# Optimization experiments

Measured on AMD Instinct MI355X. Metric: run time of the kernel, lower is better.

The kernel has to match this reference:

```python
import jax, jax.numpy as jnp
import numpy as np

NUM = 8          # nlk*nlk - 1
IDX_REF = 4      # center neighbor index


def _gather2d(img, yi, xi):
    # img: (B,H,W); yi,xi: int32 (B,K,H,W) already clipped in-range
    B, H, W = img.shape
    flat = img.reshape(B, H * W)
    idx = (yi * W + xi).reshape(B, -1)
    return jnp.take_along_axis(flat, idx, axis=1).reshape(yi.shape)


def _bilinear(img, ys, xs):
    # bilinear sample with zero padding outside (deform-conv v2 semantics)
    # img: (B,H,W); ys,xs: float (B,K,H,W)
    B, H, W = img.shape
    y0 = jnp.floor(ys)
    x0 = jnp.floor(xs)
    y0i = y0.astype(jnp.int32)
    x0i = x0.astype(jnp.int32)
    wy1 = ys - y0
    wx1 = xs - x0
    out = jnp.zeros(ys.shape, img.dtype)
    for dy, wy in ((0, 1.0 - wy1), (1, wy1)):
        for dx, wx in ((0, 1.0 - wx1), (1, wx1)):
            yy = y0i + dy
            xx = x0i + dx
            valid = ((yy >= 0) & (yy < H) & (xx >= 0) & (xx < W)).astype(img.dtype)
            v = _gather2d(img, jnp.clip(yy, 0, H - 1), jnp.clip(xx, 0, W - 1))
            out = out + wy * wx * valid * v
    return out


def _conv3(x, w):
    return jax.lax.conv_general_dilated(x, w, (1, 1), ((1, 1), (1, 1)),
                                        dimension_numbers=('NCHW', 'OIHW', 'NCHW'))


def _bn_relu(x, g, b, m, v):
    s = g / jnp.sqrt(v + 1e-5)
    return jax.nn.relu(x * s[None, :, None, None] + (b - m * s)[None, :, None, None])


def _disp_warp(right, disp):
    # sample right image at x' = x - disparity, bilinear along width, zeros outside
    B, C, H, W = right.shape
    xs = jnp.arange(W, dtype=right.dtype)[None, None, :] - disp[:, 0]  # (B,H,W)
    x0 = jnp.floor(xs)
    x0i = x0.astype(jnp.int32)
    w1 = xs - x0
    out = jnp.zeros_like(right)
    for d, w in ((0, 1.0 - w1), (1, w1)):
        xi = x0i + d
        valid = ((xi >= 0) & (xi < W)).astype(right.dtype)
        v = jnp.take_along_axis(right, jnp.clip(xi, 0, W - 1)[:, None], axis=3)
        out = out + (w * valid)[:, None] * v
    return out


def _forward(coarse_disparity, normal_estimation, left_image, right_image, confidence,
             conv1_w, bn1_g, bn1_b, bn1_m, bn1_v,
             conv2_w, bn2_g, bn2_b, bn2_m, bn2_v,
             conv3_w, aff_scale_const):
    B, _, H, W = coarse_disparity.shape
    # current_scale == 1 => interpolate is identity, disp_ == coarse_disparity
    warped_error = _disp_warp(right_image, coarse_disparity) - left_image
    guidance = jnp.concatenate([normal_estimation, left_image, right_image, warped_error], axis=1)

    x = _bn_relu(_conv3(guidance, conv1_w), bn1_g, bn1_b, bn1_m, bn1_v)
    x = _bn_relu(_conv3(x, conv2_w), bn2_g, bn2_b, bn2_m, bn2_v)
    oa = _conv3(x, conv3_w)                                   # (B, 3*NUM, H, W)

    o1, o2, aff = oa[:, :NUM], oa[:, NUM:2 * NUM], oa[:, 2 * NUM:]
    # torch: cat((o1,o2),1).view(B,NUM,2,H,W) -> faithful pairing of channels
    off = jnp.concatenate([o1, o2], axis=1).reshape(B, NUM, 2, H, W)
    zero_c = jnp.zeros((B, 1, 2, H, W), off.dtype)
    off9 = jnp.concatenate([off[:, :IDX_REF], zero_c, off[:, IDX_REF:]], axis=1)  # (B,9,2,H,W)

    aff = jnp.tanh(aff) / (aff_scale_const + 1e-8)            # TGASS

    # confidence gather at p + offset_k (1x1 deform conv, w_conf=1), offsets detached
    ii = jnp.arange(H, dtype=off.dtype)[None, None, :, None]
    jj = jnp.arange(W, dtype=off.dtype)[None, None, None, :]
    off_nc = jax.lax.stop_gradient(
        jnp.concatenate([off9[:, :IDX_REF], off9[:, IDX_REF + 1:]], axis=1))  # (B,8,2,H,W)
    conf_aff = _bilinear(confidence[:, 0], ii + off_nc[:, :, 0], jj + off_nc[:, :, 1])
    aff = aff * conf_aff

    s = jnp.sum(jnp.abs(aff), axis=1, keepdims=True) + 1e-4
    s = jnp.maximum(s, 1.0)                                   # TGASS clamp
    aff = aff / s
    aff_ref = 1.0 - jnp.sum(aff, axis=1, keepdims=True)
    aff9 = jnp.concatenate([aff[:, :IDX_REF], aff_ref, aff[:, IDX_REF:]], axis=1)  # (B,9,H,W)

    # one propagation: modulated deformable 3x3 conv, all-ones weight, zero bias
    ky = (jnp.arange(9, dtype=off.dtype) // 3 - 1.0)[None, :, None, None]
    kx = (jnp.arange(9, dtype=off.dtype) % 3 - 1.0)[None, :, None, None]
    sampled = _bilinear(coarse_disparity[:, 0], ii + ky + off9[:, :, 0], jj + kx + off9[:, :, 1])
    inter = jnp.sum(aff9 * sampled, axis=1, keepdims=True)    # (B,1,H,W)
    inter = inter * (inter >= 0).astype(inter.dtype)
    inter = jnp.maximum(inter, 0.0)
    final = jnp.maximum(0.7 * coarse_disparity + 0.3 * inter, 0.0)
    return final


def setup_inputs() -> dict:
    key = jax.random.key(0)
    ks = jax.random.split(key, 20)
    B, H, W = 4, 384, 1280
    inp = {}
    inp['coarse_disparity'] = jax.random.uniform(ks[0], (B, 1, H, W), jnp.float32) * 40.0
    inp['normal_estimation'] = jax.random.normal(ks[1], (B, 3, H, W), jnp.float32)
    inp['left_image'] = jax.random.uniform(ks[2], (B, 3, H, W), jnp.float32)
    inp['right_image'] = jax.random.uniform(ks[3], (B, 3, H, W), jnp.float32)
    inp['confidence'] = jax.random.uniform(ks[4], (B, 1, H, W), jnp.float32)
    inp['conv1_w'] = jax.random.normal(ks[5], (32, 12, 3, 3), jnp.float32) * 0.05
    inp['bn1_g'] = jax.random.uniform(ks[6], (32,), jnp.float32) + 0.5
    inp['bn1_b'] = jax.random.normal(ks[7], (32,), jnp.float32) * 0.1
    inp['bn1_m'] = jax.random.normal(ks[8], (32,), jnp.float32) * 0.1
    inp['bn1_v'] = jax.random.uniform(ks[9], (32,), jnp.float32) + 0.5
    inp['conv2_w'] = jax.random.normal(ks[10], (64, 32, 3, 3), jnp.float32) * 0.05
    inp['bn2_g'] = jax.random.uniform(ks[11], (64,), jnp.float32) + 0.5
    inp['bn2_b'] = jax.random.normal(ks[12], (64,), jnp.float32) * 0.1
    inp['bn2_m'] = jax.random.normal(ks[13], (64,), jnp.float32) * 0.1
    inp['bn2_v'] = jax.random.uniform(ks[14], (64,), jnp.float32) + 0.5
    inp['conv3_w'] = jax.random.normal(ks[15], (3 * NUM, 64, 3, 3), jnp.float32) * 0.05
    inp['aff_scale_const'] = jnp.array([1.0 * NUM], jnp.float32)  # affinity_gamma * num
    return inp


def reference(coarse_disparity, normal_estimation, left_image, right_image, confidence,
              conv1_w, bn1_g, bn1_b, bn1_m, bn1_v,
              conv2_w, bn2_g, bn2_b, bn2_m, bn2_v,
              conv3_w, aff_scale_const):
    return _forward(coarse_disparity, normal_estimation, left_image, right_image, confidence,
                    conv1_w, bn1_g, bn1_b, bn1_m, bn1_v,
                    conv2_w, bn2_g, bn2_b, bn2_m, bn2_v,
                    conv3_w, aff_scale_const)
```

## Files before the change

### kernel.cpp

```cpp
#include <hip/hip_runtime.h>
#include <math.h>

static constexpr int B_ = 4;
static constexpr int H_ = 384;
static constexpr int W_ = 1280;
static constexpr int HW_ = H_ * W_;

typedef _Float16 f16x8 __attribute__((ext_vector_type(8)));
typedef float f32x4 __attribute__((ext_vector_type(4)));


template <int C_IN, int C_OUT>
__global__ __launch_bounds__(256) void prep_w(const float* __restrict__ w,
                                              unsigned short* __restrict__ wb)
{
  constexpr int CICH = C_IN / 32;
  constexpr int NCOT = (C_OUT + 15) / 16;
  constexpr int NE = NCOT * CICH * 9 * 512;
  int i = blockIdx.x * 256 + threadIdx.x;
  if (i >= NE) return;
  int k   = i & 31;
  int row = (i >> 5) & 15;
  int ts  = i >> 9;
  int s   = ts % 9;
  int tc  = ts / 9;
  int c   = tc % CICH;
  int t   = tc / CICH;
  int co  = t * 16 + row;
  int ci  = c * 32 + k;
  float v = 0.f;
  if (co < C_OUT) v = w[((size_t)co * C_IN + ci) * 9 + s];
  union { _Float16 f; unsigned short u; } ch;
  ch.f = (_Float16)v;
  wb[i] = ch.u;
}

__global__ __launch_bounds__(256) void prep_w1(const float* __restrict__ w,
                                               unsigned short* __restrict__ wb)
{
  constexpr int NE = 2 * 6 * 512;
  int i = blockIdx.x * 256 + threadIdx.x;
  if (i >= NE) return;
  int k    = i & 31;
  int row  = (i >> 5) & 15;
  int ts   = i >> 9;
  int chunk = ts % 6;
  int tc   = ts / 6;
  int ky   = chunk >> 1;
  int kc   = chunk & 1;
  int kx, ci;
  bool valid;
  if (kc == 0) { kx = k >> 4;  ci = k & 15; valid = (ci < 12); }
  else         { kx = 2;       ci = k & 15; valid = (k < 16) && (ci < 12); }
  int co = tc * 16 + row;
  float v = valid ? w[((size_t)co * 12 + ci) * 9 + ky * 3 + kx] : 0.f;
  union { _Float16 f; unsigned short u; } ch;
  ch.f = (_Float16)v;
  wb[i] = ch.u;
}

__global__ __launch_bounds__(256, 4) void conv1_mfma(
    const float* __restrict__ disp, const float* __restrict__ normal,
    const float* __restrict__ left, const float* __restrict__ right,
    const unsigned short* __restrict__ wb,
    const float* __restrict__ bn_g, const float* __restrict__ bn_b,
    const float* __restrict__ bn_m, const float* __restrict__ bn_v,
    unsigned short* __restrict__ out,
    int b0, int out_y0, int out_rows)
{
  constexpr int NCOT = 2;
  constexpr int TY  = 8;
  constexpr int HR  = 10;
  constexpr int TXI = 36;

  __shared__ unsigned short smem[HR * TXI * 16];

  const int tilesX = W_ / 32;
  int bb = blockIdx.x;
  const int txi = bb % tilesX; bb /= tilesX;
  const int tilesY = (out_rows + TY - 1) / TY;
  const int tyi = bb % tilesY;
  const int gi  = bb / tilesY;
  const int b   = b0 + gi;
  const int x0  = txi * 32;
  const int oy0 = out_y0 + tyi * TY;

  const int tid    = threadIdx.x;
  const int w      = tid >> 6;
  const int lane15 = tid & 15;
  const int kgrp   = (tid >> 4) & 3;
  const int aoff   = lane15 * 32 + kgrp * 8;

  f32x4 acc[NCOT][2][2];
#pragma unroll
  for (int i = 0; i < NCOT; i++)
#pragma unroll
    for (int rr = 0; rr < 2; rr++) {
      acc[i][rr][0] = (f32x4){0.f, 0.f, 0.f, 0.f};
      acc[i][rr][1] = (f32x4){0.f, 0.f, 0.f, 0.f};
    }

  for (int it = tid; it < HR * TXI; it += 256) {
    int row = it / TXI;
    int px  = it - row * TXI;
    int gy  = oy0 - 1 + row;
    int gx  = x0 - 2 + px;
    union { _Float16 f[16]; uint4 u[2]; } R;
    R.u[0] = (uint4){0, 0, 0, 0};
    R.u[1] = (uint4){0, 0, 0, 0};
    if (((unsigned)gy < (unsigned)H_) & ((unsigned)gx < (unsigned)W_)) {
      size_t p = (size_t)gy * W_ + gx;
      float d = disp[(size_t)b * HW_ + p];
      float xs = (float)gx - d;
      float x0f = floorf(xs);
      int xi0 = (int)x0f;
      float w1 = xs - x0f;
      int xi1 = xi0 + 1;
      float v0 = (xi0 >= 0 && xi0 < W_) ? 1.f : 0.f;
      float v1 = (xi1 >= 0 && xi1 < W_) ? 1.f : 0.f;
      int xc0 = min(max(xi0, 0), W_ - 1);
      int xc1 = min(max(xi1, 0), W_ - 1);
      float w0f = (1.f - w1) * v0;
      float w1f = w1 * v1;
#pragma unroll
      for (int c = 0; c < 3; c++) {
        const float* rrow = right + (size_t)(b * 3 + c) * HW_ + (size_t)gy * W_;
        float l = left[(size_t)(b * 3 + c) * HW_ + p];
        float n = normal[(size_t)(b * 3 + c) * HW_ + p];
        float r = rrow[gx];
        float warped = w0f * rrow[xc0] + w1f * rrow[xc1];
        R.f[c]     = (_Float16)n;
        R.f[3 + c] = (_Float16)l;
        R.f[6 + c] = (_Float16)r;
        R.f[9 + c] = (_Float16)(warped - l);
      }
    }
    unsigned short* dst = &smem[it * 16];
    *(uint4*)(dst)     = R.u[0];
    *(uint4*)(dst + 8) = R.u[1];
  }
  __syncthreads();

  f16x8 ah[NCOT];
#pragma unroll
  for (int tc = 0; tc < NCOT; tc++)
    ah[tc] = *(const f16x8*)(wb + ((size_t)(tc * 6 + 0) * 512 + aoff));
#pragma unroll
  for (int c = 0; c < 6; c++) {
    const int ky = c >> 1, kc = c & 1;
    f16x8 ahn[NCOT];
    if (c < 5) {
#pragma unroll
      for (int tc = 0; tc < NCOT; tc++)
        ahn[tc] = *(const f16x8*)(wb + ((size_t)(tc * 6 + c + 1) * 512 + aoff));
    }
#pragma unroll
    for (int rr = 0; rr < 2; rr++) {
      const int col = (kc ? 3 : 1) + lane15;
      const int e0 = ((2 * w + rr + ky) * TXI + col) * 16 + kgrp * 8;
      f16x8 b0 = *(const f16x8*)&smem[e0];
      f16x8 b1 = *(const f16x8*)&smem[e0 + 256];
#pragma unroll
      for (int tc = 0; tc < NCOT; tc++) {
        acc[tc][rr][0] = __builtin_amdgcn_mfma_f32_16x16x32_f16(
            ah[tc], b0, acc[tc][rr][0], 0, 0, 0);
        acc[tc][rr][1] = __builtin_amdgcn_mfma_f32_16x16x32_f16(
            ah[tc], b1, acc[tc][rr][1], 0, 0, 0);
      }
    }
    if (c < 5) {
#pragma unroll
      for (int tc = 0; tc < NCOT; tc++) ah[tc] = ahn[tc];
    }
  }

#pragma unroll
  for (int rr = 0; rr < 2; rr++) {
    const int orow = oy0 + 2 * w + rr;
    if (orow < out_y0 + out_rows) {
      const int ox = x0 + lane15;
#pragma unroll
      for (int tc = 0; tc < NCOT; tc++) {
        const int o = tc * 2 + (kgrp >> 1);
        const size_t recbase =
            (((size_t)(gi * 4 + o) * out_rows + (orow - out_y0)) * W_ + ox) * 8
            + (kgrp & 1) * 4;
#pragma unroll
        for (int nt = 0; nt < 2; nt++) {
          union { _Float16 f[4]; uint2 u; } Hh;
#pragma unroll
          for (int j = 0; j < 4; j++) {
            const int co = tc * 16 + kgrp * 4 + j;
            float s = bn_g[co] * rsqrtf(bn_v[co] + 1e-5f);
            float v = fmaxf(acc[tc][rr][nt][j] * s + (bn_b[co] - bn_m[co] * s), 0.f);
            Hh.f[j] = (_Float16)v;
          }
          *(uint2*)&out[recbase + (size_t)nt * 128] = Hh.u;
        }
      }
    }
  }
}

__global__ __launch_bounds__(256, 4) void conv2_mfma(
    const unsigned short* __restrict__ in, const unsigned short* __restrict__ wb,
    const float* __restrict__ bn_g, const float* __restrict__ bn_b,
    const float* __restrict__ bn_m, const float* __restrict__ bn_v,
    unsigned short* __restrict__ out,
    int in_y0, int in_rows, int out_y0, int out_rows)
{
  constexpr int C_IN = 32, C_OUT = 64;
  constexpr int CICH = 1;
  constexpr int NCIO = 4;
  constexpr int NCOT = 4;
  constexpr int TY  = 8;
  constexpr int HR  = 10;
  constexpr int TXI = 36;
  constexpr int PX2 = 18;
  constexpr int PXW = 36;

  __shared__ unsigned short smem[HR * TXI * PXW];

  const int tilesX = W_ / 32;
  int bb = blockIdx.x;
  const int txi = bb % tilesX; bb /= tilesX;
  const int tilesY = (out_rows + TY - 1) / TY;
  const int tyi = bb % tilesY;
  const int gi  = bb / tilesY;
  const int x0  = txi * 32;
  const int oy0 = out_y0 + tyi * TY;

  const int tid    = threadIdx.x;
  const int w      = tid >> 6;
  const int lane15 = tid & 15;
  const int kgrp   = (tid >> 4) & 3;
  const int aoff   = lane15 * 32 + kgrp * 8;

  f32x4 acc[NCOT][2][2];
#pragma unroll
  for (int i = 0; i < NCOT; i++)
#pragma unroll
    for (int rr = 0; rr < 2; rr++) {
      acc[i][rr][0] = (f32x4){0.f, 0.f, 0.f, 0.f};
      acc[i][rr][1] = (f32x4){0.f, 0.f, 0.f, 0.f};
    }

  for (int it = tid; it < 4 * HR * PX2; it += 256) {
    int cib = it / (HR * PX2);
    int pos = it - cib * (HR * PX2);
    int row = pos / PX2;
    int p2  = pos - row * PX2;
    int gy  = oy0 - 1 + row;
    int by  = gy - in_y0;
    int gx  = x0 - 2 + 2 * p2;
    const bool rok = (unsigned)by < (unsigned)in_rows;
    uint4 h0 = {0,0,0,0}, h1 = {0,0,0,0};
    const unsigned short* src =
        in + (((size_t)(gi * NCIO + cib) * in_rows + by) * W_ + gx) * 8;
    if (rok & ((unsigned)gx < (unsigned)W_))       h0 = *(const uint4*)(src);
    if (rok & ((unsigned)(gx + 1) < (unsigned)W_)) h1 = *(const uint4*)(src + 8);
    int base = (row * TXI + 2 * p2) * PXW + cib * 8;
    *(uint4*)&smem[base]       = h0;
    *(uint4*)&smem[base + PXW] = h1;
  }
  __syncthreads();

  f16x8 ah[NCOT];
#pragma unroll
  for (int tc = 0; tc < NCOT; tc++)
    ah[tc] = *(const f16x8*)(wb + ((size_t)(tc * 9) * 512 + aoff));
#pragma unroll
  for (int s = 0; s < 9; s++) {
    const int ky = s / 3, kx = s - 3 * ky;
    f16x8 ahn[NCOT];
    if (s < 8) {
#pragma unroll
      for (int tc = 0; tc < NCOT; tc++)
        ahn[tc] = *(const f16x8*)(wb + ((size_t)(tc * 9 + s + 1) * 512 + aoff));
    }
#pragma unroll
    for (int rr = 0; rr < 2; rr++) {
      const int e0 = ((2 * w + rr + ky) * TXI + 1 + lane15 + kx) * PXW + kgrp * 8;
      f16x8 b0 = *(const f16x8*)&smem[e0];
      f16x8 b1 = *(const f16x8*)&smem[e0 + 16 * PXW];
#pragma unroll
      for (int tc = 0; tc < NCOT; tc++) {
        acc[tc][rr][0] = __builtin_amdgcn_mfma_f32_16x16x32_f16(
            ah[tc], b0, acc[tc][rr][0], 0, 0, 0);
        acc[tc][rr][1] = __builtin_amdgcn_mfma_f32_16x16x32_f16(
            ah[tc], b1, acc[tc][rr][1], 0, 0, 0);
      }
    }
    if (s < 8) {
#pragma unroll
      for (int tc = 0; tc < NCOT; tc++) ah[tc] = ahn[tc];
    }
  }

#pragma unroll
  for (int rr = 0; rr < 2; rr++) {
    const int orow = oy0 + 2 * w + rr;
    if (orow < out_y0 + out_rows) {
      const int ox = x0 + lane15;
#pragma unroll
      for (int tc = 0; tc < NCOT; tc++) {
        const int o = tc * 2 + (kgrp >> 1);
        const size_t recbase =
            (((size_t)(gi * 8 + o) * out_rows + (orow - out_y0)) * W_ + ox) * 8
            + (kgrp & 1) * 4;
#pragma unroll
        for (int nt = 0; nt < 2; nt++) {
          union { _Float16 f[4]; uint2 u; } Hh;
#pragma unroll
          for (int j = 0; j < 4; j++) {
            const int co = tc * 16 + kgrp * 4 + j;
            float s = bn_g[co] * rsqrtf(bn_v[co] + 1e-5f);
            float v = fmaxf(acc[tc][rr][nt][j] * s + (bn_b[co] - bn_m[co] * s), 0.f);
            Hh.f[j] = (_Float16)v;
          }
          *(uint2*)&out[recbase + (size_t)nt * 128] = Hh.u;
        }
      }
    }
  }
}

__device__ __forceinline__ float bilin1(const float* __restrict__ img,
                                        float ys, float xs)
{
  float y0f = floorf(ys), x0f = floorf(xs);
  int y0 = (int)y0f, x0 = (int)x0f;
  float wy1 = ys - y0f, wx1 = xs - x0f;
  float wy0 = 1.f - wy1, wx0 = 1.f - wx1;
  int y1 = y0 + 1, x1 = x0 + 1;
  float vy0 = (y0 >= 0 && y0 < H_) ? 1.f : 0.f;
  float vy1 = (y1 >= 0 && y1 < H_) ? 1.f : 0.f;
  float vx0 = (x0 >= 0 && x0 < W_) ? 1.f : 0.f;
  float vx1 = (x1 >= 0 && x1 < W_) ? 1.f : 0.f;
  int yc0 = min(max(y0, 0), H_ - 1), yc1 = min(max(y1, 0), H_ - 1);
  int xc0 = min(max(x0, 0), W_ - 1), xc1 = min(max(x1, 0), W_ - 1);
  const float* r0 = img + (size_t)yc0 * W_;
  const float* r1 = img + (size_t)yc1 * W_;
  float v00 = r0[xc0], v01 = r0[xc1], v10 = r1[xc0], v11 = r1[xc1];
  return (wy0 * vy0) * ((wx0 * vx0) * v00 + (wx1 * vx1) * v01) +
         (wy1 * vy1) * ((wx0 * vx0) * v10 + (wx1 * vx1) * v11);
}

__global__ __launch_bounds__(256, 4) void conv3_final(
    const unsigned short* __restrict__ in, const unsigned short* __restrict__ wb,
    const float* __restrict__ conf, const float* __restrict__ disp,
    const float* __restrict__ asc, float* __restrict__ outp,
    int b0, int in_y0, int in_rows, int out_y0, int out_rows)
{
  constexpr int NCIO = 8;
  constexpr int CICH = 2;
  constexpr int NCOT = 2;
  constexpr int TY  = 8;
  constexpr int HR  = 10;
  constexpr int TXI = 36;
  constexpr int PX2 = 18;
  constexpr int PXW = 36;
  constexpr int COS = 260;

  __shared__ unsigned short smem[HR * TXI * PXW];
  float* oal = (float*)smem;

  const int tilesX = W_ / 32;
  int bb = blockIdx.x;
  const int txi = bb % tilesX; bb /= tilesX;
  const int tilesY = (out_rows + TY - 1) / TY;
  const int tyi = bb % tilesY;
  const int gi  = bb / tilesY;
  const int b   = b0 + gi;
  const int x0  = txi * 32;
  const int oy0 = out_y0 + tyi * TY;

  const int tid    = threadIdx.x;
  const int w      = tid >> 6;
  const int lane15 = tid & 15;
  const int kgrp   = (tid >> 4) & 3;
  const int aoff   = lane15 * 32 + kgrp * 8;

  f32x4 acc[NCOT][2][2];
#pragma unroll
  for (int i = 0; i < NCOT; i++)
#pragma unroll
    for (int rr = 0; rr < 2; rr++) {
      acc[i][rr][0] = (f32x4){0.f, 0.f, 0.f, 0.f};
      acc[i][rr][1] = (f32x4){0.f, 0.f, 0.f, 0.f};
    }

  for (int cc = 0; cc < CICH; ++cc) {
    if (cc) __syncthreads();
    for (int it = tid; it < 4 * HR * PX2; it += 256) {
      int cib = it / (HR * PX2);
      int pos = it - cib * (HR * PX2);
      int row = pos / PX2;
      int p2  = pos - row * PX2;
      int gy  = oy0 - 1 + row;
      int by  = gy - in_y0;
      int gx  = x0 - 2 + 2 * p2;
      const bool rok = (unsigned)by < (unsigned)in_rows;
      uint4 h0 = {0,0,0,0}, h1 = {0,0,0,0};
      const unsigned short* src =
          in + (((size_t)(gi * NCIO + cc * 4 + cib) * in_rows + by) * W_ + gx) * 8;
      if (rok & ((unsigned)gx < (unsigned)W_))       h0 = *(const uint4*)(src);
      if (rok & ((unsigned)(gx + 1) < (unsigned)W_)) h1 = *(const uint4*)(src + 8);
      int base = (row * TXI + 2 * p2) * PXW + cib * 8;
      *(uint4*)&smem[base]       = h0;
      *(uint4*)&smem[base + PXW] = h1;
    }
    __syncthreads();

    f16x8 ah[NCOT];
#pragma unroll
    for (int tc = 0; tc < NCOT; tc++)
      ah[tc] = *(const f16x8*)(
          wb + ((size_t)((tc * CICH + cc) * 9) * 512 + aoff));
#pragma unroll
    for (int s = 0; s < 9; s++) {
      const int ky = s / 3, kx = s - 3 * ky;
      f16x8 ahn[NCOT];
      if (s < 8) {
#pragma unroll
        for (int tc = 0; tc < NCOT; tc++)
          ahn[tc] = *(const f16x8*)(
              wb + ((size_t)((tc * CICH + cc) * 9 + s + 1) * 512 + aoff));
      }
#pragma unroll
      for (int rr = 0; rr < 2; rr++) {
        const int e0 = ((2 * w + rr + ky) * TXI + 1 + lane15 + kx) * PXW + kgrp * 8;
        f16x8 b0 = *(const f16x8*)&smem[e0];
        f16x8 b1 = *(const f16x8*)&smem[e0 + 16 * PXW];
#pragma unroll
        for (int tc = 0; tc < NCOT; tc++) {
          acc[tc][rr][0] = __builtin_amdgcn_mfma_f32_16x16x32_f16(
              ah[tc], b0, acc[tc][rr][0], 0, 0, 0);
          acc[tc][rr][1] = __builtin_amdgcn_mfma_f32_16x16x32_f16(
              ah[tc], b1, acc[tc][rr][1], 0, 0, 0);
        }
      }
      if (s < 8) {
#pragma unroll
        for (int tc = 0; tc < NCOT; tc++) ah[tc] = ahn[tc];
      }
    }
  }

  __syncthreads();
#pragma unroll
  for (int tc = 0; tc < NCOT; tc++) {
#pragma unroll
    for (int j = 0; j < 4; j++) {
      const int co = tc * 16 + kgrp * 4 + j;
      if (co < 24) {
#pragma unroll
        for (int rr = 0; rr < 2; rr++) {
          const int row = 2 * w + rr;
#pragma unroll
          for (int nt = 0; nt < 2; nt++)
            oal[co * COS + row * 32 + lane15 + nt * 16] = acc[tc][rr][nt][j];
        }
      }
    }
  }
  __syncthreads();

  const int px = tid & 31;
  const int r  = tid >> 5;
  const int orow = oy0 + r;
  const int gx = x0 + px;
  if (orow < out_y0 + out_rows) {
    const float scale = 1.f / (asc[0] + 1e-8f);
    const float* cimg = conf + (size_t)b * HW_;
    const float* dimg = disp + (size_t)b * HW_;
    const int base = r * 32 + px;

    float offy[8], offx[8], a[8];
#pragma unroll
    for (int k = 0; k < 8; k++) {
      offy[k] = oal[(size_t)k * COS + base];
      offx[k] = oal[(size_t)(8 + k) * COS + base];
      float ar = oal[(size_t)(16 + k) * COS + base];
      float ca = bilin1(cimg, (float)orow + offy[k], (float)gx + offx[k]);
      a[k] = tanhf(ar) * scale * ca;
    }

    float s = 1e-4f;
#pragma unroll
    for (int k = 0; k < 8; k++) s += fabsf(a[k]);
    s = fmaxf(s, 1.f);
    float inv = 1.f / s;
    float suma = 0.f;
#pragma unroll
    for (int k = 0; k < 8; k++) { a[k] *= inv; suma += a[k]; }
    float aref = 1.f - suma;

    float inter = 0.f;
#pragma unroll
    for (int k9 = 0; k9 < 9; k9++) {
      float oy, ox, wk;
      if (k9 < 4)       { oy = offy[k9];     ox = offx[k9];     wk = a[k9]; }
      else if (k9 == 4) { oy = 0.f;          ox = 0.f;          wk = aref;  }
      else              { oy = offy[k9 - 1]; ox = offx[k9 - 1]; wk = a[k9 - 1]; }
      float ky = (float)(k9 / 3) - 1.f;
      float kx = (float)(k9 % 3) - 1.f;
      inter += wk * bilin1(dimg, (float)orow + ky + oy, (float)gx + kx + ox);
    }
    inter = fmaxf(inter, 0.f);
    float cd = dimg[(size_t)orow * W_ + gx];
    outp[(size_t)b * HW_ + (size_t)orow * W_ + gx] =
        fmaxf(0.7f * cd + 0.3f * inter, 0.f);
  }
}

extern "C" void kernel_launch(void* const* d_in, const int* in_sizes, int n_in,
                              void* d_out, int out_size, void* d_ws, size_t ws_size,
                              hipStream_t stream)
{
  const float* disp   = (const float*)d_in[0];
  const float* normal = (const float*)d_in[1];
  const float* left   = (const float*)d_in[2];
  const float* right  = (const float*)d_in[3];
  const float* conf   = (const float*)d_in[4];
  const float* w1     = (const float*)d_in[5];
  const float* g1     = (const float*)d_in[6];
  const float* b1     = (const float*)d_in[7];
  const float* m1     = (const float*)d_in[8];
  const float* v1     = (const float*)d_in[9];
  const float* w2     = (const float*)d_in[10];
  const float* g2     = (const float*)d_in[11];
  const float* b2     = (const float*)d_in[12];
  const float* m2     = (const float*)d_in[13];
  const float* v2     = (const float*)d_in[14];
  const float* w3     = (const float*)d_in[15];
  const float* asc    = (const float*)d_in[16];
  float* out = (float*)d_out;

  constexpr int WB1E = 2 * 6 * 512;
  constexpr int WB2E = 4 * 1 * 9 * 512;
  constexpr int WB3E = 2 * 2 * 9 * 512;
  const size_t wbytes = (size_t)(WB1E + WB2E + WB3E) * sizeof(unsigned short);

  struct Cfg { int g, bh; };
  const Cfg cfgs[] = {{4, 384}, {2, 384}, {1, 384}, {4, 96}, {2, 96},
                      {1, 96}, {1, 48}, {1, 24}, {1, 12}, {1, 8}, {1, 4}};
  int G = 1, BH = 4;
  for (const Cfg& c : cfgs) {
    size_t bytes = (size_t)c.g * W_ *
                   (64u * (c.bh + 4) + 128u * (c.bh + 2));
    if (bytes + wbytes <= ws_size) { G = c.g; BH = c.bh; break; }
  }

  unsigned short* x1s = (unsigned short*)d_ws;
  unsigned short* x2s = x1s + (size_t)G * 32 * (BH + 4) * W_;
  unsigned short* wb1 = x2s + (size_t)G * 64 * (BH + 2) * W_;
  unsigned short* wb2 = wb1 + WB1E;
  unsigned short* wb3 = wb2 + WB2E;

  prep_w1<<<(WB1E + 255) / 256, 256, 0, stream>>>(w1, wb1);
  prep_w<32, 64><<<(WB2E + 255) / 256, 256, 0, stream>>>(w2, wb2);
  prep_w<64, 24><<<(WB3E + 255) / 256, 256, 0, stream>>>(w3, wb3);

  const int tilesX = W_ / 32;

  for (int b0 = 0; b0 < B_; b0 += G) {
    for (int y0 = 0; y0 < H_; y0 += BH) {
      const int rows_out = min(BH, H_ - y0);
      const int y_x2_0 = max(y0 - 1, 0);
      const int y_x2_1 = min(y0 + rows_out + 1, H_);
      const int rows_x2 = y_x2_1 - y_x2_0;
      const int y_x1_0 = max(y0 - 2, 0);
      const int y_x1_1 = min(y0 + rows_out + 2, H_);
      const int rows_x1 = y_x1_1 - y_x1_0;

      {
        int grid = tilesX * ((rows_x1 + 7) / 8) * G;
        conv1_mfma<<<grid, 256, 0, stream>>>(
            disp, normal, left, right, wb1, g1, b1, m1, v1, x1s,
            b0, y_x1_0, rows_x1);
      }
      {
        int grid = tilesX * ((rows_x2 + 7) / 8) * G;
        conv2_mfma<<<grid, 256, 0, stream>>>(
            x1s, wb2, g2, b2, m2, v2, x2s,
            y_x1_0, rows_x1, y_x2_0, rows_x2);
      }
      {
        int grid = tilesX * ((rows_out + 7) / 8) * G;
        conv3_final<<<grid, 256, 0, stream>>>(
            x2s, wb3, conf, disp, asc, out,
            b0, y_x2_0, rows_x2, y0, rows_out);
      }
    }
  }
}
```

Before: 560.7 us.

## Fuse conv1 and conv2 into one kernel, keeping conv1 activations in LDS

Merges the conv1 and conv2 kernels so each block computes the conv1 output plus a halo (12x36) into shared memory, then runs conv2 from there. This removes the global write and read of the 32-channel conv1 intermediate and one kernel launch per band. In exchange, the halo rows and columns are recomputed per tile, LDS use rises, and occupancy drops to 3 blocks per CU.

```diff
diff --git a/kernel.cpp b/kernel.cpp
--- a/kernel.cpp
+++ b/kernel.cpp
@@ -59,31 +59,35 @@
   wb[i] = ch.u;
 }
 
-__global__ __launch_bounds__(256, 4) void conv1_mfma(
+__global__ __launch_bounds__(256, 3) void conv12_mfma(
     const float* __restrict__ disp, const float* __restrict__ normal,
     const float* __restrict__ left, const float* __restrict__ right,
-    const unsigned short* __restrict__ wb,
-    const float* __restrict__ bn_g, const float* __restrict__ bn_b,
-    const float* __restrict__ bn_m, const float* __restrict__ bn_v,
+    const unsigned short* __restrict__ wb1, const unsigned short* __restrict__ wb2,
+    const float* __restrict__ g1, const float* __restrict__ b1,
+    const float* __restrict__ m1, const float* __restrict__ v1,
+    const float* __restrict__ g2, const float* __restrict__ b2,
+    const float* __restrict__ m2, const float* __restrict__ v2,
     unsigned short* __restrict__ out,
     int b0, int out_y0, int out_rows)
 {
-  constexpr int NCOT = 2;
-  constexpr int TY  = 8;
-  constexpr int HR  = 10;
-  constexpr int TXI = 36;
-
-  __shared__ unsigned short smem[HR * TXI * 16];
+  constexpr int GW = 52;
+  constexpr int GR = 12;
+  constexpr int XW = 36;
+  constexpr int XR = 12;
+  constexpr int P1 = 2 * 6 * 512;
+
+  __shared__ unsigned short gmem[GR * GW * 16];
+  __shared__ unsigned short xmem[XR * XW * 36];
 
   const int tilesX = W_ / 32;
   int bb = blockIdx.x;
   const int txi = bb % tilesX; bb /= tilesX;
-  const int tilesY = (out_rows + TY - 1) / TY;
+  const int tilesY = (out_rows + 7) / 8;
   const int tyi = bb % tilesY;
   const int gi  = bb / tilesY;
   const int b   = b0 + gi;
   const int x0  = txi * 32;
-  const int oy0 = out_y0 + tyi * TY;
+  const int oy0 = out_y0 + tyi * 8;
 
   const int tid    = threadIdx.x;
   const int w      = tid >> 6;
@@ -91,20 +95,11 @@
   const int kgrp   = (tid >> 4) & 3;
   const int aoff   = lane15 * 32 + kgrp * 8;
 
-  f32x4 acc[NCOT][2][2];
-#pragma unroll
-  for (int i = 0; i < NCOT; i++)
-#pragma unroll
-    for (int rr = 0; rr < 2; rr++) {
-      acc[i][rr][0] = (f32x4){0.f, 0.f, 0.f, 0.f};
-      acc[i][rr][1] = (f32x4){0.f, 0.f, 0.f, 0.f};
-    }
-
-  for (int it = tid; it < HR * TXI; it += 256) {
-    int row = it / TXI;
-    int px  = it - row * TXI;
-    int gy  = oy0 - 1 + row;
-    int gx  = x0 - 2 + px;
+  for (int it = tid; it < GR * GW; it += 256) {
+    int g  = it / GW;
+    int cx = it - g * GW;
+    int gy = oy0 - 2 + g;
+    int gx = x0 - 3 + cx;
     union { _Float16 f[16]; uint4 u[2]; } R;
     R.u[0] = (uint4){0, 0, 0, 0};
     R.u[1] = (uint4){0, 0, 0, 0};
@@ -114,63 +109,146 @@
       float xs = (float)gx - d;
       float x0f = floorf(xs);
       int xi0 = (int)x0f;
-      float w1 = xs - x0f;
+      float w1f_ = xs - x0f;
       int xi1 = xi0 + 1;
-      float v0 = (xi0 >= 0 && xi0 < W_) ? 1.f : 0.f;
-      float v1 = (xi1 >= 0 && xi1 < W_) ? 1.f : 0.f;
+      float vv0 = (xi0 >= 0 && xi0 < W_) ? 1.f : 0.f;
+      float vv1 = (xi1 >= 0 && xi1 < W_) ? 1.f : 0.f;
       int xc0 = min(max(xi0, 0), W_ - 1);
       int xc1 = min(max(xi1, 0), W_ - 1);
-      float w0f = (1.f - w1) * v0;
-      float w1f = w1 * v1;
+      float w0f = (1.f - w1f_) * vv0;
+      float w1f2 = w1f_ * vv1;
 #pragma unroll
       for (int c = 0; c < 3; c++) {
         const float* rrow = right + (size_t)(b * 3 + c) * HW_ + (size_t)gy * W_;
         float l = left[(size_t)(b * 3 + c) * HW_ + p];
         float n = normal[(size_t)(b * 3 + c) * HW_ + p];
         float r = rrow[gx];
-        float warped = w0f * rrow[xc0] + w1f * rrow[xc1];
+        float warped = w0f * rrow[xc0] + w1f2 * rrow[xc1];
         R.f[c]     = (_Float16)n;
         R.f[3 + c] = (_Float16)l;
         R.f[6 + c] = (_Float16)r;
         R.f[9 + c] = (_Float16)(warped - l);
       }
     }
-    unsigned short* dst = &smem[it * 16];
+    unsigned short* dst = &gmem[it * 16];
     *(uint4*)(dst)     = R.u[0];
     *(uint4*)(dst + 8) = R.u[1];
   }
   __syncthreads();
 
-  f16x8 ah[NCOT];
-#pragma unroll
-  for (int tc = 0; tc < NCOT; tc++)
-    ah[tc] = *(const f16x8*)(wb + ((size_t)(tc * 6 + 0) * 512 + aoff));
-#pragma unroll
-  for (int c = 0; c < 6; c++) {
-    const int ky = c >> 1, kc = c & 1;
-    f16x8 ahn[NCOT];
-    if (c < 5) {
-#pragma unroll
-      for (int tc = 0; tc < NCOT; tc++)
-        ahn[tc] = *(const f16x8*)(wb + ((size_t)(tc * 6 + c + 1) * 512 + aoff));
-    }
+  {
+    f32x4 a1[2][3][3];
+#pragma unroll
+    for (int tc = 0; tc < 2; tc++)
+#pragma unroll
+      for (int r = 0; r < 3; r++)
+#pragma unroll
+        for (int nt = 0; nt < 3; nt++)
+          a1[tc][r][nt] = (f32x4){0.f, 0.f, 0.f, 0.f};
+
+    f16x8 ah[2];
+#pragma unroll
+    for (int tc = 0; tc < 2; tc++)
+      ah[tc] = *(const f16x8*)(wb1 + ((size_t)(tc * 6 + 0) * 512 + aoff));
+#pragma unroll
+    for (int c = 0; c < 6; c++) {
+      const int ky = c >> 1, kc = c & 1;
+      f16x8 ahn[2];
+      if (c < 5) {
+#pragma unroll
+        for (int tc = 0; tc < 2; tc++)
+          ahn[tc] = *(const f16x8*)(wb1 + ((size_t)(tc * 6 + c + 1) * 512 + aoff));
+      }
+#pragma unroll
+      for (int r = 0; r < 3; r++) {
+        const int s = 3 * w + r;
+        const int g = min(max(s + ky - 1, 0), GR - 1);
+#pragma unroll
+        for (int nt = 0; nt < 3; nt++) {
+          const int col = nt * 16 + lane15 + (kc ? 2 : 0);
+          const int e = (g * GW + col) * 16 + kgrp * 8;
+          f16x8 bf = *(const f16x8*)&gmem[e];
+#pragma unroll
+          for (int tc = 0; tc < 2; tc++)
+            a1[tc][r][nt] = __builtin_amdgcn_mfma_f32_16x16x32_f16(
+                ah[tc], bf, a1[tc][r][nt], 0, 0, 0);
+        }
+      }
+      if (c < 5) {
+#pragma unroll
+        for (int tc = 0; tc < 2; tc++) ah[tc] = ahn[tc];
+      }
+    }
+
+    __syncthreads();
+#pragma unroll
+    for (int tc = 0; tc < 2; tc++) {
+#pragma unroll
+      for (int j = 0; j < 4; j++) {
+        const int co = tc * 16 + kgrp * 4 + j;
+        float sc = g1[co] * rsqrtf(v1[co] + 1e-5f);
+        float of = b1[co] - m1[co] * sc;
+#pragma unroll
+        for (int r = 0; r < 3; r++) {
+          const int s = 3 * w + r;
+          const int gyr = oy0 - 2 + s;
+          const bool rowok = (unsigned)gyr < (unsigned)H_;
+#pragma unroll
+          for (int nt = 0; nt < 3; nt++) {
+            const int o = nt * 16 + lane15;
+            if (o < XW) {
+              const int gx2 = x0 - 2 + o;
+              const bool ok = rowok & ((unsigned)gx2 < (unsigned)W_);
+              float v = ok ? fmaxf(a1[tc][r][nt][j] * sc + of, 0.f) : 0.f;
+              union { _Float16 f; unsigned short u; } cv;
+              cv.f = (_Float16)v;
+              xmem[(s * XW + o) * 36 + co] = cv.u;
+            }
+          }
+        }
+      }
+    }
+  }
+  __syncthreads();
+
+  f32x4 acc[4][2][2];
+#pragma unroll
+  for (int i = 0; i < 4; i++)
 #pragma unroll
     for (int rr = 0; rr < 2; rr++) {
-      const int col = (kc ? 3 : 1) + lane15;
-      const int e0 = ((2 * w + rr + ky) * TXI + col) * 16 + kgrp * 8;
-      f16x8 b0 = *(const f16x8*)&smem[e0];
-      f16x8 b1 = *(const f16x8*)&smem[e0 + 256];
-#pragma unroll
-      for (int tc = 0; tc < NCOT; tc++) {
+      acc[i][rr][0] = (f32x4){0.f, 0.f, 0.f, 0.f};
+      acc[i][rr][1] = (f32x4){0.f, 0.f, 0.f, 0.f};
+    }
+
+  f16x8 ah2[4];
+#pragma unroll
+  for (int tc = 0; tc < 4; tc++)
+    ah2[tc] = *(const f16x8*)(wb2 + ((size_t)(tc * 9) * 512 + aoff));
+#pragma unroll
+  for (int s = 0; s < 9; s++) {
+    const int ky = s / 3, kx = s - 3 * ky;
+    f16x8 ahn2[4];
+    if (s < 8) {
+#pragma unroll
+      for (int tc = 0; tc < 4; tc++)
+        ahn2[tc] = *(const f16x8*)(wb2 + ((size_t)(tc * 9 + s + 1) * 512 + aoff));
+    }
+#pragma unroll
+    for (int rr = 0; rr < 2; rr++) {
+      const int e0 = ((2 * w + rr + ky + 1) * XW + 1 + lane15 + kx) * 36 + kgrp * 8;
+      f16x8 bb0 = *(const f16x8*)&xmem[e0];
+      f16x8 bb1 = *(const f16x8*)&xmem[e0 + 16 * 36];
+#pragma unroll
+      for (int tc = 0; tc < 4; tc++) {
         acc[tc][rr][0] = __builtin_amdgcn_mfma_f32_16x16x32_f16(
-            ah[tc], b0, acc[tc][rr][0], 0, 0, 0);
+            ah2[tc], bb0, acc[tc][rr][0], 0, 0, 0);
         acc[tc][rr][1] = __builtin_amdgcn_mfma_f32_16x16x32_f16(
-            ah[tc], b1, acc[tc][rr][1], 0, 0, 0);
-      }
-    }
-    if (c < 5) {
-#pragma unroll
-      for (int tc = 0; tc < NCOT; tc++) ah[tc] = ahn[tc];
+            ah2[tc], bb1, acc[tc][rr][1], 0, 0, 0);
+      }
+    }
+    if (s < 8) {
+#pragma unroll
+      for (int tc = 0; tc < 4; tc++) ah2[tc] = ahn2[tc];
     }
   }
 
@@ -180,130 +258,7 @@
     if (orow < out_y0 + out_rows) {
       const int ox = x0 + lane15;
 #pragma unroll
-      for (int tc = 0; tc < NCOT; tc++) {
-        const int o = tc * 2 + (kgrp >> 1);
-        const size_t recbase =
-            (((size_t)(gi * 4 + o) * out_rows + (orow - out_y0)) * W_ + ox) * 8
-            + (kgrp & 1) * 4;
-#pragma unroll
-        for (int nt = 0; nt < 2; nt++) {
-          union { _Float16 f[4]; uint2 u; } Hh;
-#pragma unroll
-          for (int j = 0; j < 4; j++) {
-            const int co = tc * 16 + kgrp * 4 + j;
-            float s = bn_g[co] * rsqrtf(bn_v[co] + 1e-5f);
-            float v = fmaxf(acc[tc][rr][nt][j] * s + (bn_b[co] - bn_m[co] * s), 0.f);
-            Hh.f[j] = (_Float16)v;
-          }
-          *(uint2*)&out[recbase + (size_t)nt * 128] = Hh.u;
-        }
-      }
-    }
-  }
-}
-
-__global__ __launch_bounds__(256, 4) void conv2_mfma(
-    const unsigned short* __restrict__ in, const unsigned short* __restrict__ wb,
-    const float* __restrict__ bn_g, const float* __restrict__ bn_b,
-    const float* __restrict__ bn_m, const float* __restrict__ bn_v,
-    unsigned short* __restrict__ out,
-    int in_y0, int in_rows, int out_y0, int out_rows)
-{
-  constexpr int C_IN = 32, C_OUT = 64;
-  constexpr int CICH = 1;
-  constexpr int NCIO = 4;
-  constexpr int NCOT = 4;
-  constexpr int TY  = 8;
-  constexpr int HR  = 10;
-  constexpr int TXI = 36;
-  constexpr int PX2 = 18;
-  constexpr int PXW = 36;
-
-  __shared__ unsigned short smem[HR * TXI * PXW];
-
-  const int tilesX = W_ / 32;
-  int bb = blockIdx.x;
-  const int txi = bb % tilesX; bb /= tilesX;
-  const int tilesY = (out_rows + TY - 1) / TY;
-  const int tyi = bb % tilesY;
-  const int gi  = bb / tilesY;
-  const int x0  = txi * 32;
-  const int oy0 = out_y0 + tyi * TY;
-
-  const int tid    = threadIdx.x;
-  const int w      = tid >> 6;
-  const int lane15 = tid & 15;
-  const int kgrp   = (tid >> 4) & 3;
-  const int aoff   = lane15 * 32 + kgrp * 8;
-
-  f32x4 acc[NCOT][2][2];
-#pragma unroll
-  for (int i = 0; i < NCOT; i++)
-#pragma unroll
-    for (int rr = 0; rr < 2; rr++) {
-      acc[i][rr][0] = (f32x4){0.f, 0.f, 0.f, 0.f};
-      acc[i][rr][1] = (f32x4){0.f, 0.f, 0.f, 0.f};
-    }
-
-  for (int it = tid; it < 4 * HR * PX2; it += 256) {
-    int cib = it / (HR * PX2);
-    int pos = it - cib * (HR * PX2);
-    int row = pos / PX2;
-    int p2  = pos - row * PX2;
-    int gy  = oy0 - 1 + row;
-    int by  = gy - in_y0;
-    int gx  = x0 - 2 + 2 * p2;
-    const bool rok = (unsigned)by < (unsigned)in_rows;
-    uint4 h0 = {0,0,0,0}, h1 = {0,0,0,0};
-    const unsigned short* src =
-        in + (((size_t)(gi * NCIO + cib) * in_rows + by) * W_ + gx) * 8;
-    if (rok & ((unsigned)gx < (unsigned)W_))       h0 = *(const uint4*)(src);
-    if (rok & ((unsigned)(gx + 1) < (unsigned)W_)) h1 = *(const uint4*)(src + 8);
-    int base = (row * TXI + 2 * p2) * PXW + cib * 8;
-    *(uint4*)&smem[base]       = h0;
-    *(uint4*)&smem[base + PXW] = h1;
-  }
-  __syncthreads();
-
-  f16x8 ah[NCOT];
-#pragma unroll
-  for (int tc = 0; tc < NCOT; tc++)
-    ah[tc] = *(const f16x8*)(wb + ((size_t)(tc * 9) * 512 + aoff));
-#pragma unroll
-  for (int s = 0; s < 9; s++) {
-    const int ky = s / 3, kx = s - 3 * ky;
-    f16x8 ahn[NCOT];
-    if (s < 8) {
-#pragma unroll
-      for (int tc = 0; tc < NCOT; tc++)
-        ahn[tc] = *(const f16x8*)(wb + ((size_t)(tc * 9 + s + 1) * 512 + aoff));
-    }
-#pragma unroll
-    for (int rr = 0; rr < 2; rr++) {
-      const int e0 = ((2 * w + rr + ky) * TXI + 1 + lane15 + kx) * PXW + kgrp * 8;
-      f16x8 b0 = *(const f16x8*)&smem[e0];
-      f16x8 b1 = *(const f16x8*)&smem[e0 + 16 * PXW];
-#pragma unroll
-      for (int tc = 0; tc < NCOT; tc++) {
-        acc[tc][rr][0] = __builtin_amdgcn_mfma_f32_16x16x32_f16(
-            ah[tc], b0, acc[tc][rr][0], 0, 0, 0);
-        acc[tc][rr][1] = __builtin_amdgcn_mfma_f32_16x16x32_f16(
-            ah[tc], b1, acc[tc][rr][1], 0, 0, 0);
-      }
-    }
-    if (s < 8) {
-#pragma unroll
-      for (int tc = 0; tc < NCOT; tc++) ah[tc] = ahn[tc];
-    }
-  }
-
-#pragma unroll
-  for (int rr = 0; rr < 2; rr++) {
-    const int orow = oy0 + 2 * w + rr;
-    if (orow < out_y0 + out_rows) {
-      const int ox = x0 + lane15;
-#pragma unroll
-      for (int tc = 0; tc < NCOT; tc++) {
+      for (int tc = 0; tc < 4; tc++) {
         const int o = tc * 2 + (kgrp >> 1);
         const size_t recbase =
             (((size_t)(gi * 8 + o) * out_rows + (orow - out_y0)) * W_ + ox) * 8
@@ -314,8 +269,8 @@
 #pragma unroll
           for (int j = 0; j < 4; j++) {
             const int co = tc * 16 + kgrp * 4 + j;
-            float s = bn_g[co] * rsqrtf(bn_v[co] + 1e-5f);
-            float v = fmaxf(acc[tc][rr][nt][j] * s + (bn_b[co] - bn_m[co] * s), 0.f);
+            float sc = g2[co] * rsqrtf(v2[co] + 1e-5f);
+            float v = fmaxf(acc[tc][rr][nt][j] * sc + (b2[co] - m2[co] * sc), 0.f);
             Hh.f[j] = (_Float16)v;
           }
           *(uint2*)&out[recbase + (size_t)nt * 128] = Hh.u;
@@ -547,13 +502,11 @@
                       {1, 96}, {1, 48}, {1, 24}, {1, 12}, {1, 8}, {1, 4}};
   int G = 1, BH = 4;
   for (const Cfg& c : cfgs) {
-    size_t bytes = (size_t)c.g * W_ *
-                   (64u * (c.bh + 4) + 128u * (c.bh + 2));
+    size_t bytes = (size_t)c.g * W_ * (128u * (c.bh + 2));
     if (bytes + wbytes <= ws_size) { G = c.g; BH = c.bh; break; }
   }
 
-  unsigned short* x1s = (unsigned short*)d_ws;
-  unsigned short* x2s = x1s + (size_t)G * 32 * (BH + 4) * W_;
+  unsigned short* x2s = (unsigned short*)d_ws;
   unsigned short* wb1 = x2s + (size_t)G * 64 * (BH + 2) * W_;
   unsigned short* wb2 = wb1 + WB1E;
   unsigned short* wb3 = wb2 + WB2E;
@@ -570,21 +523,13 @@
       const int y_x2_0 = max(y0 - 1, 0);
       const int y_x2_1 = min(y0 + rows_out + 1, H_);
       const int rows_x2 = y_x2_1 - y_x2_0;
-      const int y_x1_0 = max(y0 - 2, 0);
-      const int y_x1_1 = min(y0 + rows_out + 2, H_);
-      const int rows_x1 = y_x1_1 - y_x1_0;
-
-      {
-        int grid = tilesX * ((rows_x1 + 7) / 8) * G;
-        conv1_mfma<<<grid, 256, 0, stream>>>(
-            disp, normal, left, right, wb1, g1, b1, m1, v1, x1s,
-            b0, y_x1_0, rows_x1);
-      }
+
       {
         int grid = tilesX * ((rows_x2 + 7) / 8) * G;
-        conv2_mfma<<<grid, 256, 0, stream>>>(
-            x1s, wb2, g2, b2, m2, v2, x2s,
-            y_x1_0, rows_x1, y_x2_0, rows_x2);
+        conv12_mfma<<<grid, 256, 0, stream>>>(
+            disp, normal, left, right, wb1, wb2,
+            g1, b1, m1, v1, g2, b2, m2, v2, x2s,
+            b0, y_x2_0, rows_x2);
       }
       {
         int grid = tilesX * ((rows_out + 7) / 8) * G;
```

After: 584.0 us. 4.2% more time.
